# Optimization experiments

Hardware: AMD Instinct MI355X
Metric: run time of the kernel (lower is better)

## Reference

```python
import jax, jax.numpy as jnp
import numpy as np

RATIO = 1.0 / 32  # spacial_ratio
HOUT = 7          # pooled_h
WOUT = 7          # pooled_w
S = 2             # sub_bin_size = int(sqrt(n_sampled=4))


def setup_inputs() -> dict:
    key = jax.random.key(0)
    k1, k2, k3, k4, k5, k6 = jax.random.split(key, 6)
    B, C, H, W = 4, 256, 50, 50
    N = 1024
    img_w, img_h = W / RATIO, H / RATIO
    features = jax.random.normal(k1, (B, C, H, W), dtype=jnp.float32)
    b = jax.random.randint(k2, (N,), 0, B).astype(jnp.float32)
    x1 = jax.random.uniform(k3, (N,), minval=0.0, maxval=img_w - 232.0)
    y1 = jax.random.uniform(k4, (N,), minval=0.0, maxval=img_h - 232.0)
    bw = jax.random.uniform(k5, (N,), minval=32.0, maxval=232.0)
    bh = jax.random.uniform(k6, (N,), minval=32.0, maxval=232.0)
    rois = jnp.stack([b, x1, y1, x1 + bw, y1 + bh], axis=1)  # [N, 5]
    return {"features": features, "rois": rois}


def _roi_align(features, rois):
    B, C, H, W = features.shape
    fW = jnp.float32(W)
    fH = jnp.float32(H)
    b_idx = rois[:, 0].astype(jnp.int32)            # [N]
    box = rois[:, 1:] * RATIO                       # [N, 4] in feature coords
    bx1 = jnp.clip(box[:, 0], 0.0, fW)
    by1 = jnp.clip(box[:, 1], 0.0, fH)
    bx2 = jnp.clip(box[:, 2], 0.0, fW)
    by2 = jnp.clip(box[:, 3], 0.0, fH)
    roi_valid = (bx2 - bx1 > 0) & (by2 - by1 > 0)   # [N]
    bin_w = (bx2 - bx1) / WOUT                      # [N]
    bin_h = (by2 - by1) / HOUT

    jj = jnp.arange(WOUT, dtype=jnp.float32)
    ii = jnp.arange(HOUT, dtype=jnp.float32)
    # bin edges; y2/x2 computed from the UNclamped start, then clamped (matches original order)
    x1u = bx1[:, None] + jj * bin_w[:, None]        # [N, WOUT]
    x2b = jnp.clip(x1u + bin_w[:, None], 0.0, fW)
    x1b = jnp.clip(x1u, 0.0, fW)
    y1u = by1[:, None] + ii * bin_h[:, None]        # [N, HOUT]
    y2b = jnp.clip(y1u + bin_h[:, None], 0.0, fH)
    y1b = jnp.clip(y1u, 0.0, fH)
    bin_valid = (y2b > y1b)[:, :, None] & (x2b > x1b)[:, None, :]  # [N, HOUT, WOUT]

    # SxS sample-point centers inside each bin (sub_bin = bin / S, center offset 0.5)
    cc = jnp.arange(S, dtype=jnp.float32) + 0.5
    px = x1b[:, :, None] + cc * (bin_w / S)[:, None, None]  # [N, WOUT, S]
    py = y1b[:, :, None] + cc * (bin_h / S)[:, None, None]  # [N, HOUT, S]

    xl = jnp.clip(jnp.floor(px), 0, W - 1).astype(jnp.int32)
    xh = jnp.clip(xl + 1, 0, W - 1)
    yl = jnp.clip(jnp.floor(py), 0, H - 1).astype(jnp.int32)
    yh = jnp.clip(yl + 1, 0, H - 1)
    wxh = px - xl  # (x - x1)
    wxl = xh - px  # (x2 - x)
    wyb = py - yl  # (y - y1)
    wyt = yh - py  # (y2 - y)

    feats = features.transpose(0, 2, 3, 1)          # [B, H, W, C]
    bI = b_idx[:, None, None, None, None]           # [N,1,1,1,1]
    # x varies over (WOUT, sx) -> broadcast axes (2,4); y over (HOUT, sy) -> axes (1,3)
    XL = xl[:, None, :, None, :]
    XH = xh[:, None, :, None, :]
    YL = yl[:, :, None, :, None]
    YH = yh[:, :, None, :, None]
    WXh = wxh[:, None, :, None, :, None]
    WXl = wxl[:, None, :, None, :, None]
    WYb = wyb[:, :, None, :, None, None]
    WYt = wyt[:, :, None, :, None, None]

    v_tl = feats[bI, YL, XL]   # [N, HOUT, WOUT, S, S, C]
    v_tr = feats[bI, YL, XH]
    v_bl = feats[bI, YH, XL]
    v_br = feats[bI, YH, XH]
    top = WXh * v_tr + WXl * v_tl
    bot = WXh * v_br + WXl * v_bl
    val = WYb * bot + WYt * top                     # [N, HOUT, WOUT, S, S, C]

    pooled = val.max(axis=(3, 4))                   # max over sample grid -> [N, HOUT, WOUT, C]
    mask = bin_valid & roi_valid[:, None, None]
    pooled = jnp.where(mask[..., None], pooled, 0.0)
    return pooled.transpose(0, 3, 1, 2)             # [N, C, HOUT, WOUT]


def reference(features, rois):
    return _roi_align(features, rois)
```

## Files before the change

### kernel.cpp

```cpp
#include <hip/hip_runtime.h>


namespace {

constexpr int B_ = 4, C_ = 256, H_ = 50, W_ = 50;
constexpr int HW = H_ * W_;
constexpr int HO = 7, WO = 7, NBIN = HO * WO;
constexpr int OUT_PER_ROI = C_ * NBIN;
constexpr int LD = 257;
constexpr float RATIO = 1.0f / 32.0f;

__device__ __forceinline__ unsigned short f2b(float x)
{
    unsigned u = __float_as_uint(x);
    u += 0x7fffu + ((u >> 16) & 1u);
    return (unsigned short)(u >> 16);
}

__device__ __forceinline__ float4 b2f(const uint2 r)
{
    float4 o;
    o.x = __uint_as_float(r.x << 16);
    o.y = __uint_as_float(r.x & 0xffff0000u);
    o.z = __uint_as_float(r.y << 16);
    o.w = __uint_as_float(r.y & 0xffff0000u);
    return o;
}

__global__ __launch_bounds__(256) void transpose_tiled(
    const float* __restrict__ f, unsigned short* __restrict__ ft)
{
    __shared__ float tile[64][65];
    const int bt   = blockIdx.x;
    const int hw_t = bt % 40;
    const int c_t  = (bt / 40) % 4;
    const int b    = bt / 160;
    const int hw0 = hw_t * 64, c0 = c_t * 64;
    const int lx = threadIdx.x & 63;
    const int ly = threadIdx.x >> 6;

#pragma unroll
    for (int k = 0; k < 16; ++k) {
        const int c  = c0 + k * 4 + ly;
        const int hw = hw0 + lx;
        if (hw < HW)
            tile[k * 4 + ly][lx] = f[((size_t)b * C_ + c) * HW + hw];
    }
    __syncthreads();
#pragma unroll
    for (int k = 0; k < 16; ++k) {
        const int hw = hw0 + k * 4 + ly;
        if (hw < HW)
            ft[((size_t)b * HW + hw) * C_ + c0 + lx] = f2b(tile[lx][k * 4 + ly]);
    }
}

template<int AX, int AY>
__device__ __forceinline__ float4 bin_max(const float4 p[3][3],
                                          const float4 wa, const float4 wb)
{
    float4 s[2][2];
#pragma unroll
    for (int sy = 0; sy < 2; ++sy) {
#pragma unroll
        for (int sx = 0; sx < 2; ++sx) {
            const int xk = AX * sx, yj = AY * sy;
            const float wxh = sx ? wa.y : wa.x;
            const float wxl = sx ? wa.w : wa.z;
            const float wyb = sy ? wb.y : wb.x;
            const float wyt = sy ? wb.w : wb.z;
            const float4 tl = p[yj][xk],     tr = p[yj][xk + 1];
            const float4 bl = p[yj + 1][xk], br = p[yj + 1][xk + 1];
            float4 o;
            o.x = wyb * (wxh * br.x + wxl * bl.x) + wyt * (wxh * tr.x + wxl * tl.x);
            o.y = wyb * (wxh * br.y + wxl * bl.y) + wyt * (wxh * tr.y + wxl * tl.y);
            o.z = wyb * (wxh * br.z + wxl * bl.z) + wyt * (wxh * tr.z + wxl * tl.z);
            o.w = wyb * (wxh * br.w + wxl * bl.w) + wyt * (wxh * tr.w + wxl * tl.w);
            s[sy][sx] = o;
        }
    }
    float4 m;
    m.x = fmaxf(fmaxf(s[0][0].x, s[0][1].x), fmaxf(s[1][0].x, s[1][1].x));
    m.y = fmaxf(fmaxf(s[0][0].y, s[0][1].y), fmaxf(s[1][0].y, s[1][1].y));
    m.z = fmaxf(fmaxf(s[0][0].z, s[0][1].z), fmaxf(s[1][0].z, s[1][1].z));
    m.w = fmaxf(fmaxf(s[0][0].w, s[0][1].w), fmaxf(s[1][0].w, s[1][1].w));
    return m;
}

template<int AX, int AY>
__device__ __forceinline__ float4 do_bin(const uint2* __restrict__ pb2,
                                         const unsigned o[9],
                                         const float4 wa, const float4 wb)
{
    float4 p[3][3];
#pragma unroll
    for (int j = 0; j < 2 + AY; ++j)
#pragma unroll
        for (int k = 0; k < 2 + AX; ++k)
            p[j][k] = b2f(pb2[(int)o[j * 3 + k] << 6]);
    return bin_max<AX, AY>(p, wa, wb);
}

__global__ __launch_bounds__(512, 6) void roialign_main(
    const unsigned short* __restrict__ ft,
    const float* __restrict__ rois,
    float* __restrict__ out)
{
    __shared__ float stage[NBIN * LD];
    __shared__ __align__(16) float    wts[NBIN][8];
    __shared__ __align__(16) unsigned offp[NBIN][12];

    const int n    = blockIdx.x;
    const int tid  = threadIdx.x;
    const int wave = tid >> 6;
    const int lane = tid & 63;
    const float fW = (float)W_, fH = (float)H_;

    if (tid < NBIN) {
        const int ii = tid / WO, jj = tid % WO;
        const float* r = rois + n * 5;
        const float bx1 = fminf(fmaxf(r[1] * RATIO, 0.0f), fW);
        const float by1 = fminf(fmaxf(r[2] * RATIO, 0.0f), fH);
        const float bx2 = fminf(fmaxf(r[3] * RATIO, 0.0f), fW);
        const float by2 = fminf(fmaxf(r[4] * RATIO, 0.0f), fH);
        const bool roi_valid = (bx2 - bx1 > 0.0f) && (by2 - by1 > 0.0f);
        const float bin_w = (bx2 - bx1) * (1.0f / (float)WO);
        const float bin_h = (by2 - by1) * (1.0f / (float)HO);

        const float x1u = bx1 + (float)jj * bin_w;
        const float x1b = fminf(fmaxf(x1u, 0.0f), fW);
        const float x2b = fminf(fmaxf(x1u + bin_w, 0.0f), fW);
        const float y1u = by1 + (float)ii * bin_h;
        const float y1b = fminf(fmaxf(y1u, 0.0f), fH);
        const float y2b = fminf(fmaxf(y1u + bin_h, 0.0f), fH);
        const float vf = (roi_valid && (y2b > y1b) && (x2b > x1b)) ? 1.0f : 0.0f;

        int xl[2], yl[2];
#pragma unroll
        for (int s = 0; s < 2; ++s) {
            const float px = x1b + ((float)s + 0.5f) * (bin_w * 0.5f);
            int l = (int)floorf(px);
            l = min(max(l, 0), W_ - 1);
            const int h = min(l + 1, W_ - 1);
            xl[s] = l;
            wts[tid][0 + s] = vf * (px - (float)l);
            wts[tid][2 + s] = vf * ((float)h - px);

            const float py = y1b + ((float)s + 0.5f) * (bin_h * 0.5f);
            int t = (int)floorf(py);
            t = min(max(t, 0), H_ - 1);
            const int u = min(t + 1, H_ - 1);
            yl[s] = t;
            wts[tid][4 + s] = py - (float)t;
            wts[tid][6 + s] = (float)u - py;
        }
        const int X0 = xl[0], Y0 = yl[0];
        const int ax = min(xl[1] - X0, 1);
        const int ay = min(yl[1] - Y0, 1);
        const int px_[3] = {X0, min(X0 + 1, W_ - 1), min(X0 + 2, W_ - 1)};
        const int py_[3] = {Y0, min(Y0 + 1, H_ - 1), min(Y0 + 2, H_ - 1)};
#pragma unroll
        for (int j = 0; j < 3; ++j)
#pragma unroll
            for (int k = 0; k < 3; ++k)
                offp[tid][j * 3 + k] = (unsigned)(py_[j] * W_ + px_[k]);
        offp[tid][9]  = (unsigned)(ax | (ay << 1));
        offp[tid][10] = 0u;
        offp[tid][11] = 0u;
    }

    int b = (int)rois[n * 5];
    b = min(max(b, 0), B_ - 1);
    const uint2* pb2 = (const uint2*)(ft + (size_t)b * HW * C_) + lane;

    __syncthreads();

#pragma unroll
    for (int i = 0; i < 7; ++i) {
        const int bin = wave + 8 * i;
        if (bin < NBIN) {
            const float4 wa = *(const float4*)wts[bin];
            const float4 wb = *(const float4*)(wts[bin] + 4);
            const uint4 o0 = *(const uint4*)&offp[bin][0];
            const uint4 o1 = *(const uint4*)&offp[bin][4];
            const uint2 o2 = *(const uint2*)&offp[bin][8];
            const unsigned o[9] = {o0.x, o0.y, o0.z, o0.w,
                                   o1.x, o1.y, o1.z, o1.w, o2.x};

            float4 m;
            switch (o2.y) {
                case 0u:  m = do_bin<0, 0>(pb2, o, wa, wb); break;
                case 1u:  m = do_bin<1, 0>(pb2, o, wa, wb); break;
                case 2u:  m = do_bin<0, 1>(pb2, o, wa, wb); break;
                default:  m = do_bin<1, 1>(pb2, o, wa, wb); break;
            }

            float* sp = &stage[bin * LD + 4 * lane];
            sp[0] = m.x; sp[1] = m.y; sp[2] = m.z; sp[3] = m.w;
        }
    }
    __syncthreads();

    float* outn = out + (size_t)n * OUT_PER_ROI;
    for (int k = tid; k < OUT_PER_ROI; k += 512) {
        const int ch  = k / NBIN;
        const int bin = k - ch * NBIN;
        outn[k] = stage[bin * LD + ch];
    }
}

}

extern "C" void kernel_launch(void* const* d_in, const int* in_sizes, int n_in,
                              void* d_out, int out_size, void* d_ws, size_t ws_size,
                              hipStream_t stream)
{
    const float* feats = (const float*)d_in[0];
    const float* rois  = (const float*)d_in[1];
    float* out = (float*)d_out;
    const int N = in_sizes[1] / 5;
    unsigned short* ft = (unsigned short*)d_ws;

    hipLaunchKernelGGL(transpose_tiled, dim3(B_ * 4 * 40), dim3(256), 0, stream,
                       feats, ft);
    hipLaunchKernelGGL(roialign_main, dim3(N), dim3(512), 0, stream,
                       ft, rois, out);
}
```

Baseline: 94.79 us.

## Stage pooled results as bf16 in LDS and widen output stores

The per-ROI LDS staging buffer now holds bf16 values instead of fp32, roughly halving shared memory per block, and the launch bound's minimum-blocks hint rises from 6 to 8 to allow more resident blocks. Output writes become float2 stores of two consecutive elements. The bin-case flag is made wave-uniform with readfirstlane, and bf16 decoding is deferred so raw gathered values stay packed in registers. The cost is a second bf16 rounding of the output values, which adds error, plus some extra index arithmetic in the write loop.

```diff
diff --git a/kernel.cpp b/kernel.cpp
--- a/kernel.cpp
+++ b/kernel.cpp
@@ -7,7 +7,7 @@
 constexpr int HW = H_ * W_;
 constexpr int HO = 7, WO = 7, NBIN = HO * WO;
 constexpr int OUT_PER_ROI = C_ * NBIN;
-constexpr int LD = 257;
+constexpr int LDH = 262;
 constexpr float RATIO = 1.0f / 32.0f;
 
 __device__ __forceinline__ unsigned short f2b(float x)
@@ -56,12 +56,20 @@
 }
 
 template<int AX, int AY>
-__device__ __forceinline__ float4 bin_max(const float4 p[3][3],
-                                          const float4 wa, const float4 wb)
-{
-    float4 s[2][2];
-#pragma unroll
-    for (int sy = 0; sy < 2; ++sy) {
+__device__ __forceinline__ float4 do_bin(const uint2* __restrict__ pb2,
+                                         const unsigned o[9],
+                                         const float4 wa, const float4 wb)
+{
+    uint2 c[3][3];
+#pragma unroll
+    for (int j = 0; j < 2 + AY; ++j)
+#pragma unroll
+        for (int k = 0; k < 2 + AX; ++k)
+            c[j][k] = pb2[(int)o[j * 3 + k] << 6];
+
+    float4 m;
+#pragma unroll
+    for (int sy = 0; sy < 2; ++sy)
 #pragma unroll
         for (int sx = 0; sx < 2; ++sx) {
             const int xk = AX * sx, yj = AY * sy;
@@ -69,44 +77,31 @@
             const float wxl = sx ? wa.w : wa.z;
             const float wyb = sy ? wb.y : wb.x;
             const float wyt = sy ? wb.w : wb.z;
-            const float4 tl = p[yj][xk],     tr = p[yj][xk + 1];
-            const float4 bl = p[yj + 1][xk], br = p[yj + 1][xk + 1];
-            float4 o;
-            o.x = wyb * (wxh * br.x + wxl * bl.x) + wyt * (wxh * tr.x + wxl * tl.x);
-            o.y = wyb * (wxh * br.y + wxl * bl.y) + wyt * (wxh * tr.y + wxl * tl.y);
-            o.z = wyb * (wxh * br.z + wxl * bl.z) + wyt * (wxh * tr.z + wxl * tl.z);
-            o.w = wyb * (wxh * br.w + wxl * bl.w) + wyt * (wxh * tr.w + wxl * tl.w);
-            s[sy][sx] = o;
+            const float4 tl = b2f(c[yj][xk]),     tr = b2f(c[yj][xk + 1]);
+            const float4 bl = b2f(c[yj + 1][xk]), br = b2f(c[yj + 1][xk + 1]);
+            float4 s;
+            s.x = wyb * (wxh * br.x + wxl * bl.x) + wyt * (wxh * tr.x + wxl * tl.x);
+            s.y = wyb * (wxh * br.y + wxl * bl.y) + wyt * (wxh * tr.y + wxl * tl.y);
+            s.z = wyb * (wxh * br.z + wxl * bl.z) + wyt * (wxh * tr.z + wxl * tl.z);
+            s.w = wyb * (wxh * br.w + wxl * bl.w) + wyt * (wxh * tr.w + wxl * tl.w);
+            if (sy == 0 && sx == 0) {
+                m = s;
+            } else {
+                m.x = fmaxf(m.x, s.x);
+                m.y = fmaxf(m.y, s.y);
+                m.z = fmaxf(m.z, s.z);
+                m.w = fmaxf(m.w, s.w);
+            }
         }
-    }
-    float4 m;
-    m.x = fmaxf(fmaxf(s[0][0].x, s[0][1].x), fmaxf(s[1][0].x, s[1][1].x));
-    m.y = fmaxf(fmaxf(s[0][0].y, s[0][1].y), fmaxf(s[1][0].y, s[1][1].y));
-    m.z = fmaxf(fmaxf(s[0][0].z, s[0][1].z), fmaxf(s[1][0].z, s[1][1].z));
-    m.w = fmaxf(fmaxf(s[0][0].w, s[0][1].w), fmaxf(s[1][0].w, s[1][1].w));
     return m;
 }
 
-template<int AX, int AY>
-__device__ __forceinline__ float4 do_bin(const uint2* __restrict__ pb2,
-                                         const unsigned o[9],
-                                         const float4 wa, const float4 wb)
-{
-    float4 p[3][3];
-#pragma unroll
-    for (int j = 0; j < 2 + AY; ++j)
-#pragma unroll
-        for (int k = 0; k < 2 + AX; ++k)
-            p[j][k] = b2f(pb2[(int)o[j * 3 + k] << 6]);
-    return bin_max<AX, AY>(p, wa, wb);
-}
-
-__global__ __launch_bounds__(512, 6) void roialign_main(
+__global__ __launch_bounds__(512, 8) void roialign_main(
     const unsigned short* __restrict__ ft,
     const float* __restrict__ rois,
     float* __restrict__ out)
 {
-    __shared__ float stage[NBIN * LD];
+    __shared__ unsigned short stageh[NBIN * LDH];
     __shared__ __align__(16) float    wts[NBIN][8];
     __shared__ __align__(16) unsigned offp[NBIN][12];
 
@@ -175,6 +170,7 @@
 
     __syncthreads();
 
+    unsigned* const st32 = (unsigned*)stageh;
 #pragma unroll
     for (int i = 0; i < 7; ++i) {
         const int bin = wave + 8 * i;
@@ -186,26 +182,36 @@
             const uint2 o2 = *(const uint2*)&offp[bin][8];
             const unsigned o[9] = {o0.x, o0.y, o0.z, o0.w,
                                    o1.x, o1.y, o1.z, o1.w, o2.x};
+            const unsigned flags = __builtin_amdgcn_readfirstlane(o2.y);
 
             float4 m;
-            switch (o2.y) {
+            switch (flags) {
                 case 0u:  m = do_bin<0, 0>(pb2, o, wa, wb); break;
                 case 1u:  m = do_bin<1, 0>(pb2, o, wa, wb); break;
                 case 2u:  m = do_bin<0, 1>(pb2, o, wa, wb); break;
                 default:  m = do_bin<1, 1>(pb2, o, wa, wb); break;
             }
 
-            float* sp = &stage[bin * LD + 4 * lane];
-            sp[0] = m.x; sp[1] = m.y; sp[2] = m.z; sp[3] = m.w;
+            const unsigned lo = (unsigned)f2b(m.x) | ((unsigned)f2b(m.y) << 16);
+            const unsigned hi = (unsigned)f2b(m.z) | ((unsigned)f2b(m.w) << 16);
+            const int di = bin * (LDH / 2) + 2 * lane;
+            st32[di]     = lo;
+            st32[di + 1] = hi;
         }
     }
     __syncthreads();
 
     float* outn = out + (size_t)n * OUT_PER_ROI;
-    for (int k = tid; k < OUT_PER_ROI; k += 512) {
-        const int ch  = k / NBIN;
-        const int bin = k - ch * NBIN;
-        outn[k] = stage[bin * LD + ch];
+    for (int t = tid; t < OUT_PER_ROI / 2; t += 512) {
+        const int k    = 2 * t;
+        const int ch   = k / NBIN;
+        const int bin  = k - ch * NBIN;
+        const int ch2  = (bin + 1 < NBIN) ? ch : ch + 1;
+        const int bin2 = (bin + 1 < NBIN) ? bin + 1 : 0;
+        float2 v;
+        v.x = __uint_as_float((unsigned)stageh[bin  * LDH + ch ] << 16);
+        v.y = __uint_as_float((unsigned)stageh[bin2 * LDH + ch2] << 16);
+        *(float2*)&outn[k] = v;
     }
 }
 
```

Result: faster. 90.00 us (-5.1%).
